# Performance work log

Hardware: AMD Instinct MI355X
Metric: run time of the kernel (lower is better)

Reference implementation:

```python
import jax, jax.numpy as jnp
import numpy as np

B, K, V, D, T = 8, 4, 32000, 1024, 16
EOS, PAD = 2, 0
EOS_SCORE = 1000.0
BIG = 1e9  # suppresses beams 1..K-1 at step 0 (original starts from a single beam)


def setup_inputs() -> dict:
    key = jax.random.key(0)
    k1, k2, k3, k4 = jax.random.split(key, 4)
    s = 1.0 / np.sqrt(D)
    return {
        "words": jnp.ones((B, K), dtype=jnp.int32),  # BOS=1 on every beam
        "h0": jnp.zeros((B, K, D), dtype=jnp.float32),
        "c0": jnp.zeros((B, K, D), dtype=jnp.float32),
        "E": jax.random.normal(k1, (V, D), dtype=jnp.float32) * s,
        "Wx": jax.random.normal(k2, (D, 4 * D), dtype=jnp.float32) * s,
        "Wh": jax.random.normal(k3, (D, 4 * D), dtype=jnp.float32) * s,
        "b": jnp.zeros((4 * D,), dtype=jnp.float32),
        "Wout": jax.random.normal(k4, (D, V), dtype=jnp.float32) * s,
        "bout": jnp.zeros((V,), dtype=jnp.float32),
    }


def reference(words, h0, c0, E, Wx, Wh, b, Wout, bout):
    bidx = jnp.arange(B)[:, None]
    kidx = jnp.arange(K)[None, :]
    scores0 = jnp.concatenate(
        [jnp.zeros((B, 1), jnp.float32), jnp.full((B, K - 1), BIG, jnp.float32)], axis=1)
    buf0 = jnp.zeros((B, K, T), dtype=jnp.int32)
    stopped0 = jnp.zeros((B,), dtype=bool)

    def step(carry, j):
        w, scores, h, c, stopped, buf = carry
        # proc_word: embed -> LSTM cell -> vocab logits (vectorized over B*K beams)
        x = E[w]                                              # [B,K,D]
        gates = jnp.einsum('bkd,df->bkf', x, Wx) + jnp.einsum('bkd,df->bkf', h, Wh) + b
        i_, f_, g_, o_ = jnp.split(gates, 4, axis=-1)
        c_new = jax.nn.sigmoid(f_) * c + jax.nn.sigmoid(i_) * jnp.tanh(g_)
        h_new = jax.nn.sigmoid(o_) * jnp.tanh(c_new)
        logits = jnp.einsum('bkd,dv->bkv', h_new, Wout) + bout  # [B,K,V]
        p = -jax.nn.log_softmax(logits, axis=-1)                # negative log-probs
        neg_ps, idxs = jax.lax.top_k(-p, K)                     # K smallest per beam
        cand = (-neg_ps) + scores[:, :, None]                   # [B,K,K]
        flat = cand.reshape(B, K * K)
        wflat = idxs.reshape(B, K * K)
        neg_sel, sel = jax.lax.top_k(-flat, K)                  # K smallest over all cands
        sel_scores = -neg_sel                                   # [B,K]
        prev = sel // K                                         # originating beam
        new_w = jnp.take_along_axis(wflat, sel, axis=1)
        eos = new_w == EOS
        first_eos = eos[:, 0] & (~stopped)                      # best cand is EOS -> stop
        pen = eos & (~first_eos[:, None]) & (~stopped[:, None]) # non-best EOS penalized
        sel_scores = jnp.where(pen, EOS_SCORE, sel_scores)
        tok = jnp.where(first_eos[:, None], EOS, new_w)
        tok = jnp.where(stopped[:, None], PAD, tok)
        prevb = jnp.where(stopped[:, None], kidx, prev)         # stopped rows keep order
        buf = buf[bidx, prevb]                                  # reorder beam histories
        buf = buf.at[:, :, j].set(tok.astype(jnp.int32))
        h_new = h_new[bidx, prev]                               # gather per-beam states
        c_new = c_new[bidx, prev]
        scores = jnp.where(stopped[:, None], scores, sel_scores)
        w = jnp.where(stopped[:, None], w, new_w.astype(w.dtype))
        stopped = stopped | first_eos
        return (w, scores, h_new, c_new, stopped, buf), None

    carry0 = (words, scores0, h0, c0, stopped0, buf0)
    (_, scores, _, _, _, buf), _ = jax.lax.scan(step, carry0, jnp.arange(T))
    return buf, scores
```

## Files before the change

### kernel.cpp

```cpp
#include <hip/hip_runtime.h>
#include <math.h>
#include <float.h>

namespace {

constexpr int Bb = 8, Kk = 4, BKn = 32, Dd = 1024, Ff = 4096, Vv = 32000, Tt = 16;
constexpr int GDS = 32, GDC = 32;
constexpr int LTW = 64;
constexpr int LNB = Vv / LTW;
constexpr int LCH = 32;
constexpr int LNCHH = 16;
constexpr int NVCH = LNB;
constexpr int EOSt = 2, PADt = 0;
constexpr float BIGf = 1e9f, EOSSf = 1000.0f;

constexpr size_t OFF_HTN = 0;
constexpr size_t OFF_CB0 = OFF_HTN + (size_t)Dd * BKn;
constexpr size_t OFF_CB1 = OFF_CB0 + (size_t)BKn * Dd;
constexpr size_t OFF_GP  = OFF_CB1 + (size_t)BKn * Dd;
constexpr size_t OFF_CS  = OFF_GP  + (size_t)GDS * BKn * Ff;
constexpr size_t OFF_SC  = OFF_CS  + (size_t)NVCH * BKn * 12;
constexpr size_t OFF_INT = OFF_SC  + BKn;
constexpr int IW = 0, ISTOP = 32, IPREV = 40, IBUFA = 72, IBUFB = IBUFA + Bb * Kk * Tt;

__device__ __forceinline__ void cp16(const float* g, float* l) {
  __builtin_amdgcn_global_load_lds(
      (const __attribute__((address_space(1))) void*)g,
      (__attribute__((address_space(3))) void*)l, 16, 0, 0);
}

__device__ inline void ins4(float v, int id, float tv[4], int ti[4]) {
#pragma unroll
  for (int r = 0; r < 4; r++) {
    bool better = (v > tv[r]) || (v == tv[r] && id < ti[r]);
    if (better) { float fv = tv[r]; int fi = ti[r]; tv[r] = v; ti[r] = id; v = fv; id = fi; }
  }
}

template <int STARTOFF>
__device__ inline void merge_top4(float tv[4], int ti[4], float ov[4], int oi[4]) {
#pragma unroll
  for (int r = 0; r < 4; r++) {
    float hv = tv[0]; int hi = ti[0];
    float m = hv;
    for (int off = STARTOFF; off; off >>= 1) m = fmaxf(m, __shfl_xor(m, off));
    int c = (hv == m) ? hi : 0x7fffffff;
    for (int off = STARTOFF; off; off >>= 1) c = min(c, __shfl_xor(c, off));
    if (hv == m && hi == c) {
      tv[0] = tv[1]; ti[0] = ti[1];
      tv[1] = tv[2]; ti[1] = ti[2];
      tv[2] = tv[3]; ti[2] = ti[3];
      tv[3] = -FLT_MAX; ti[3] = 0x7fffffff;
    }
    ov[r] = m; oi[r] = c;
  }
}

__global__ __launch_bounds__(256) void initK(const int* __restrict__ words,
    const float* __restrict__ h0, const float* __restrict__ c0,
    float* __restrict__ ws) {
  int* wsi = (int*)(ws + OFF_INT);
  if (blockIdx.x < 128) {
    int g = blockIdx.x * 256 + threadIdx.x;
    int d = g >> 5, bk = g & 31;
    ws[OFF_HTN + g] = h0[(size_t)bk * Dd + d];
    ws[OFF_CB0 + g] = c0[g];
  } else {
    int t = threadIdx.x;
    if (t < BKn) {
      ws[OFF_SC + t] = ((t & 3) == 0) ? 0.f : BIGf;
      wsi[IW + t] = words[t];
      wsi[IPREV + t] = t & 3;
    }
    if (t < Bb) wsi[ISTOP + t] = 0;
    for (int i = t; i < 2 * Bb * Kk * Tt; i += 256) wsi[IBUFA + i] = 0;
  }
}

__global__ __launch_bounds__(256) void gatesK(const float* __restrict__ Wx,
    const float* __restrict__ Wh, const float* __restrict__ E,
    const float* __restrict__ hTn, const int* __restrict__ wsi,
    float* __restrict__ Gp) {
  __shared__ float xs[GDC][BKn], hs[GDC][BKn];
  int tid = threadIdx.x;
  int d0 = blockIdx.y * GDC;
  {
    int bk = tid & 31, dq = tid >> 5;
    int w = wsi[IW + bk];
    int src = (bk & ~3) | wsi[IPREV + bk];
    const float* Erow = E + (size_t)w * Dd + d0;
#pragma unroll
    for (int k = 0; k < 4; k++) {
      int d = dq * 4 + k;
      xs[d][bk] = Erow[d];
      hs[d][bk] = hTn[(size_t)(d0 + d) * BKn + src];
    }
  }
  __syncthreads();
  int ct = tid & 31, bg = tid >> 5;
  int f0 = blockIdx.x * 128 + ct * 4;
  float acc[4][4];
#pragma unroll
  for (int c = 0; c < 4; c++)
#pragma unroll
    for (int i = 0; i < 4; i++) acc[c][i] = 0.f;
#pragma unroll 4
  for (int d = 0; d < GDC; ++d) {
    float4 wx = *(const float4*)(Wx + (size_t)(d0 + d) * Ff + f0);
    float4 wh = *(const float4*)(Wh + (size_t)(d0 + d) * Ff + f0);
    float4 x4 = *(const float4*)&xs[d][bg * 4];
    float4 h4 = *(const float4*)&hs[d][bg * 4];
    float xv[4] = {x4.x, x4.y, x4.z, x4.w};
    float hv[4] = {h4.x, h4.y, h4.z, h4.w};
    float wxc[4] = {wx.x, wx.y, wx.z, wx.w};
    float whc[4] = {wh.x, wh.y, wh.z, wh.w};
#pragma unroll
    for (int c = 0; c < 4; c++)
#pragma unroll
      for (int i = 0; i < 4; i++)
        acc[c][i] = fmaf(xv[i], wxc[c], fmaf(hv[i], whc[c], acc[c][i]));
  }
#pragma unroll
  for (int i = 0; i < 4; i++) {
    int bk = bg * 4 + i;
    float4 o = {acc[0][i], acc[1][i], acc[2][i], acc[3][i]};
    *(float4*)(Gp + ((size_t)blockIdx.y * BKn + bk) * Ff + f0) = o;
  }
}

__global__ __launch_bounds__(256) void lstmK(const float* __restrict__ bvec,
    const float* __restrict__ Gp, const float* __restrict__ cPrev,
    const int* __restrict__ wsi, float* __restrict__ cNew,
    float* __restrict__ hTn) {
  __shared__ float part[4][128];
  int bk = blockIdx.x;
  int dcl = threadIdx.x & 127;
  int half = threadIdx.x >> 7;
  int dc = blockIdx.y * 128 + dcl;
  float s[4] = {0.f, 0.f, 0.f, 0.f};
#pragma unroll 4
  for (int dsl = 0; dsl < 16; dsl++) {
    int ds = half * 16 + dsl;
    const float* row = Gp + ((size_t)ds * BKn + bk) * Ff;
#pragma unroll
    for (int g = 0; g < 4; g++) s[g] += row[(size_t)g * Dd + dc];
  }
  if (half == 1) {
#pragma unroll
    for (int g = 0; g < 4; g++) part[g][dcl] = s[g];
  }
  __syncthreads();
  if (half == 0) {
    float gi = s[0] + part[0][dcl] + bvec[dc];
    float gf = s[1] + part[1][dcl] + bvec[Dd + dc];
    float gg = s[2] + part[2][dcl] + bvec[2 * Dd + dc];
    float go = s[3] + part[3][dcl] + bvec[3 * Dd + dc];
    int src = (bk & ~3) | wsi[IPREV + bk];
    float c = cPrev[(size_t)src * Dd + dc];
    float si = 1.f / (1.f + expf(-gi));
    float sf = 1.f / (1.f + expf(-gf));
    float so = 1.f / (1.f + expf(-go));
    float tg = tanhf(gg);
    float cn = sf * c + si * tg;
    float hn = so * tanhf(cn);
    cNew[(size_t)bk * Dd + dc] = cn;
    hTn[(size_t)dc * BKn + bk] = hn;
  }
}

__global__ __launch_bounds__(256) void logitsAK(const float* __restrict__ Wo,
    const float* __restrict__ bo, const float* __restrict__ hTn,
    float* __restrict__ cs) {
  __shared__ float wb[2][3][LCH][LTW];
  __shared__ float hb[2][3][LCH][BKn];
  __shared__ float sd[BKn][LTW];
  int tid = threadIdx.x;
  int half = tid >> 7;
  int htid = tid & 127;
  int hw = htid >> 6;
  int lane = tid & 63;
  int cg = htid & 15;
  int bg = htid >> 4;
  size_t v0 = (size_t)blockIdx.x * LTW;
  int dh0 = half * 512;
  float acc[4][4];
#pragma unroll
  for (int c = 0; c < 4; c++)
#pragma unroll
    for (int i = 0; i < 4; i++) acc[c][i] = 0.f;

  float4 b4 = *(const float4*)(bo + v0 + cg * 4);

#define STAGE(CH, B)                                                           \
  {                                                                            \
    int d0_ = dh0 + (CH) * LCH;                                                \
    _Pragma("unroll") for (int i_ = 0; i_ < 4; i_++) {                         \
      int db_ = hw * 16 + i_ * 4;                                              \
      cp16(Wo + (size_t)(d0_ + db_ + (lane >> 4)) * Vv + v0 + (lane & 15) * 4, \
           &wb[half][B][db_][0]);                                              \
    }                                                                          \
    _Pragma("unroll") for (int j_ = 0; j_ < 2; j_++) {                         \
      int db_ = hw * 16 + j_ * 8;                                              \
      cp16(hTn + (size_t)(d0_ + db_ + (lane >> 3)) * BKn + (lane & 7) * 4,     \
           &hb[half][B][db_][0]);                                              \
    }                                                                          \
  }

  STAGE(0, 0)
  STAGE(1, 1)
  for (int k = 0; k < LNCHH; k++) {
    int b = k % 3;
    if (k + 2 < LNCHH) {
      STAGE(k + 2, (k + 2) % 3)
      asm volatile("s_waitcnt vmcnt(12)" ::: "memory");
    } else if (k + 1 < LNCHH) {
      asm volatile("s_waitcnt vmcnt(6)" ::: "memory");
    } else {
      asm volatile("s_waitcnt vmcnt(0)" ::: "memory");
    }
    __builtin_amdgcn_s_barrier();
#pragma unroll 8
    for (int d = 0; d < LCH; d++) {
      float4 w4 = *(const float4*)&wb[half][b][d][cg * 4];
      float4 h4 = *(const float4*)&hb[half][b][d][bg * 4];
      acc[0][0] = fmaf(w4.x, h4.x, acc[0][0]);
      acc[1][0] = fmaf(w4.y, h4.x, acc[1][0]);
      acc[2][0] = fmaf(w4.z, h4.x, acc[2][0]);
      acc[3][0] = fmaf(w4.w, h4.x, acc[3][0]);
      acc[0][1] = fmaf(w4.x, h4.y, acc[0][1]);
      acc[1][1] = fmaf(w4.y, h4.y, acc[1][1]);
      acc[2][1] = fmaf(w4.z, h4.y, acc[2][1]);
      acc[3][1] = fmaf(w4.w, h4.y, acc[3][1]);
      acc[0][2] = fmaf(w4.x, h4.z, acc[0][2]);
      acc[1][2] = fmaf(w4.y, h4.z, acc[1][2]);
      acc[2][2] = fmaf(w4.z, h4.z, acc[2][2]);
      acc[3][2] = fmaf(w4.w, h4.z, acc[3][2]);
      acc[0][3] = fmaf(w4.x, h4.w, acc[0][3]);
      acc[1][3] = fmaf(w4.y, h4.w, acc[1][3]);
      acc[2][3] = fmaf(w4.z, h4.w, acc[2][3]);
      acc[3][3] = fmaf(w4.w, h4.w, acc[3][3]);
    }
    __builtin_amdgcn_s_barrier();
  }
#undef STAGE

  if (half == 0) {
#pragma unroll
    for (int c = 0; c < 4; c++)
#pragma unroll
      for (int i = 0; i < 4; i++)
        sd[bg * 4 + i][cg * 4 + c] = acc[c][i] + ((const float*)&b4)[c];
  }
  __syncthreads();
  if (half == 1) {
#pragma unroll
    for (int c = 0; c < 4; c++)
#pragma unroll
      for (int i = 0; i < 4; i++)
        sd[bg * 4 + i][cg * 4 + c] += acc[c][i];
  }
  __syncthreads();

  int wid = tid >> 6;
  int i0 = (int)v0 + lane;
  for (int bb_ = 0; bb_ < 8; ++bb_) {
    int bk = wid * 8 + bb_;
    float v0f = sd[bk][lane];
    float m = v0f;
    for (int off = 32; off; off >>= 1) m = fmaxf(m, __shfl_xor(m, off));
    float se = expf(v0f - m);
    for (int off = 32; off; off >>= 1) se += __shfl_xor(se, off);
    float tv[4]; int ti[4];
#pragma unroll
    for (int r = 0; r < 4; r++) { tv[r] = -FLT_MAX; ti[r] = 0x7fffffff; }
    ins4(v0f, i0, tv, ti);
    float ov[4]; int oi[4];
    merge_top4<32>(tv, ti, ov, oi);
    if (lane == 0) {
      float* p = cs + ((size_t)blockIdx.x * BKn + bk) * 12;
      p[0] = m; p[1] = se;
#pragma unroll
      for (int r = 0; r < 4; r++) { p[2 + r] = ov[r]; p[6 + r] = __int_as_float(oi[r]); }
    }
  }
}

__global__ __launch_bounds__(1024) void redSelK(float* __restrict__ ws, int step) {
  __shared__ float bt_s[BKn][8];
  __shared__ int s_tok[BKn], s_prevb[BKn];
  int* wsi = (int*)(ws + OFF_INT);
  const float* cs = ws + OFF_CS;
  int tid = threadIdx.x;
  int wv = tid >> 6, lane = tid & 63;
  {
    int half = lane >> 5, l32 = lane & 31;
    int bk = wv * 2 + half;
    float tv[4]; int ti[4];
#pragma unroll
    for (int r = 0; r < 4; r++) { tv[r] = -FLT_MAX; ti[r] = 0x7fffffff; }
    float M = -FLT_MAX, ls = 0.f;
    for (int g = 0; g < 4; g++) {
      float4 pa[4], pb[4], pc[4];
      bool vv[4];
#pragma unroll
      for (int j = 0; j < 4; j++) {
        int c = l32 + 32 * (g * 4 + j);
        vv[j] = c < NVCH;
        const float* p = cs + ((size_t)c * BKn + bk) * 12;
        if (vv[j]) {
          pa[j] = *(const float4*)p;
          pb[j] = *(const float4*)(p + 4);
          pc[j] = *(const float4*)(p + 8);
        }
      }
#pragma unroll
      for (int j = 0; j < 4; j++) {
        if (vv[j]) {
          float cm = pa[j].x, csum = pa[j].y;
          if (cm > M) { ls *= expf(M - cm); M = cm; }
          ls += csum * expf(cm - M);
          ins4(pa[j].z, __float_as_int(pb[j].z), tv, ti);
          ins4(pa[j].w, __float_as_int(pb[j].w), tv, ti);
          ins4(pb[j].x, __float_as_int(pc[j].x), tv, ti);
          ins4(pb[j].y, __float_as_int(pc[j].y), tv, ti);
        }
      }
    }
    for (int off = 16; off; off >>= 1) {
      float Mo = __shfl_xor(M, off), lso = __shfl_xor(ls, off);
      float Mn = fmaxf(M, Mo);
      ls = ls * expf(M - Mn) + lso * expf(Mo - Mn);
      M = Mn;
    }
    float lse = M + logf(ls);
    float ov[4]; int oi[4];
    merge_top4<16>(tv, ti, ov, oi);
    if (l32 == 0) {
#pragma unroll
      for (int r = 0; r < 4; r++) {
        bt_s[bk][r] = lse - ov[r];
        bt_s[bk][4 + r] = __int_as_float(oi[r]);
      }
    }
  }
  __syncthreads();
  if (tid < Bb) {
    int b = tid;
    int st = wsi[ISTOP + b];
    float sc[4];
#pragma unroll
    for (int k = 0; k < 4; k++) sc[k] = ws[OFF_SC + b * 4 + k];
    float cval[16]; int ctok[16];
#pragma unroll
    for (int kb = 0; kb < 4; kb++)
#pragma unroll
      for (int r = 0; r < 4; r++) {
        cval[kb * 4 + r] = bt_s[b * 4 + kb][r] + sc[kb];
        ctok[kb * 4 + r] = __float_as_int(bt_s[b * 4 + kb][4 + r]);
      }
    float selS[4]; int selW[4], prevK[4];
    int usedMask = 0;
#pragma unroll
    for (int r = 0; r < 4; r++) {
      int best = -1; float bv = FLT_MAX;
#pragma unroll
      for (int t = 0; t < 16; t++) {
        if (!((usedMask >> t) & 1) && cval[t] < bv) { bv = cval[t]; best = t; }
      }
      usedMask |= 1 << best;
      int tok = 0;
#pragma unroll
      for (int t = 0; t < 16; t++) if (t == best) tok = ctok[t];
      selS[r] = bv; selW[r] = tok; prevK[r] = best >> 2;
    }
    bool eos[4];
#pragma unroll
    for (int r = 0; r < 4; r++) eos[r] = (selW[r] == EOSt);
    bool first = eos[0] && !st;
#pragma unroll
    for (int r = 0; r < 4; r++) if (eos[r] && !first && !st) selS[r] = EOSSf;
#pragma unroll
    for (int k = 0; k < 4; k++) {
      int tok = st ? PADt : (first ? EOSt : selW[k]);
      int pb  = st ? k : prevK[k];
      s_tok[b * 4 + k] = tok;
      s_prevb[b * 4 + k] = pb;
      if (!st) { ws[OFF_SC + b * 4 + k] = selS[k]; wsi[IW + b * 4 + k] = selW[k]; }
      wsi[IPREV + b * 4 + k] = prevK[k];
    }
    wsi[ISTOP + b] = (st || first) ? 1 : 0;
  }
  __syncthreads();
  if (tid < 512) {
    const int* br = wsi + (((step & 1) == 0) ? IBUFA : IBUFB);
    int* bw = wsi + (((step & 1) == 0) ? IBUFB : IBUFA);
    int bkk = tid >> 4, t = tid & 15;
    int pb = s_prevb[bkk];
    int src = ((bkk & ~3) | pb) * Tt + t;
    int val = br[src];
    if (t == step) val = s_tok[bkk];
    bw[tid] = val;
  }
}

__global__ __launch_bounds__(256) void outK(const float* __restrict__ ws,
                                            float* __restrict__ out) {
  const int* wsi = (const int*)(ws + OFF_INT);
  int g = blockIdx.x * 256 + threadIdx.x;
  if (g < Bb * Kk * Tt) {
    out[g] = (float)wsi[IBUFA + g];
  } else if (g < Bb * Kk * Tt + BKn) {
    out[g] = ws[OFF_SC + (g - Bb * Kk * Tt)];
  }
}

}

extern "C" void kernel_launch(void* const* d_in, const int* in_sizes, int n_in,
                              void* d_out, int out_size, void* d_ws, size_t ws_size,
                              hipStream_t stream) {
  (void)in_sizes; (void)n_in; (void)out_size; (void)ws_size;
  const int*   words = (const int*)d_in[0];
  const float* h0 = (const float*)d_in[1];
  const float* c0 = (const float*)d_in[2];
  const float* E  = (const float*)d_in[3];
  const float* Wx = (const float*)d_in[4];
  const float* Wh = (const float*)d_in[5];
  const float* bv = (const float*)d_in[6];
  const float* Wo = (const float*)d_in[7];
  const float* bo = (const float*)d_in[8];
  float* ws = (float*)d_ws;
  float* hTn = ws + OFF_HTN;
  float* cb0 = ws + OFF_CB0;
  float* cb1 = ws + OFF_CB1;
  float* Gp  = ws + OFF_GP;
  float* cs  = ws + OFF_CS;
  int*   wsi = (int*)(ws + OFF_INT);

  initK<<<129, 256, 0, stream>>>(words, h0, c0, ws);
  for (int j = 0; j < Tt; j++) {
    float* cPrev = (j & 1) ? cb1 : cb0;
    float* cNext = (j & 1) ? cb0 : cb1;
    gatesK<<<dim3(32, GDS), 256, 0, stream>>>(Wx, Wh, E, hTn, wsi, Gp);
    lstmK<<<dim3(32, 8), 256, 0, stream>>>(bv, Gp, cPrev, wsi, cNext, hTn);
    logitsAK<<<LNB, 256, 0, stream>>>(Wo, bo, hTn, cs);
    redSelK<<<1, 1024, 0, stream>>>(ws, j);
  }
  outK<<<3, 256, 0, stream>>>(ws, (float*)d_out);
}
```

Baseline: 1.780 ms.

## Repack Wout into per-tile contiguous blocks for logits kernel loads

```diff
diff --git a/kernel.cpp b/kernel.cpp
--- a/kernel.cpp
+++ b/kernel.cpp
@@ -22,6 +22,7 @@
 constexpr size_t OFF_SC  = OFF_CS  + (size_t)NVCH * BKn * 12;
 constexpr size_t OFF_INT = OFF_SC  + BKn;
 constexpr int IW = 0, ISTOP = 32, IPREV = 40, IBUFA = 72, IBUFB = IBUFA + Bb * Kk * Tt;
+constexpr size_t OFF_PWO = OFF_INT + 2048;
 
 __device__ __forceinline__ void cp16(const float* g, float* l) {
   __builtin_amdgcn_global_load_lds(
@@ -77,6 +78,33 @@
   }
 }
 
+__global__ __launch_bounds__(256) void packWoK(const float* __restrict__ Wo,
+                                               float* __restrict__ pwo) {
+  __shared__ float tile[32][256];
+  int t = threadIdx.x;
+  int v0 = blockIdx.x * 256;
+  int d0 = blockIdx.y * 32;
+  int rs = t >> 6;
+  int lane = t & 63;
+#pragma unroll
+  for (int p = 0; p < 8; p++) {
+    int r = p * 4 + rs;
+    *(float4*)&tile[r][lane * 4] =
+        *(const float4*)(Wo + (size_t)(d0 + r) * Vv + v0 + lane * 4);
+  }
+  __syncthreads();
+  int tb = rs;
+  int b = (v0 >> 6) + tb;
+  float* dst = pwo + ((size_t)b * Dd + d0) * 64;
+#pragma unroll
+  for (int p = 0; p < 8; p++) {
+    int off = p * 256 + lane * 4;
+    int dd = off >> 6;
+    int cc = off & 63;
+    *(float4*)(dst + off) = *(const float4*)&tile[dd][tb * 64 + cc];
+  }
+}
+
 __global__ __launch_bounds__(256) void gatesK(const float* __restrict__ Wx,
     const float* __restrict__ Wh, const float* __restrict__ E,
     const float* __restrict__ hTn, const int* __restrict__ wsi,
@@ -168,7 +196,7 @@
   }
 }
 
-__global__ __launch_bounds__(256) void logitsAK(const float* __restrict__ Wo,
+__global__ __launch_bounds__(256) void logitsAK(const float* __restrict__ pwo,
     const float* __restrict__ bo, const float* __restrict__ hTn,
     float* __restrict__ cs) {
   __shared__ float wb[2][3][LCH][LTW];
@@ -183,6 +211,7 @@
   int bg = htid >> 4;
   size_t v0 = (size_t)blockIdx.x * LTW;
   int dh0 = half * 512;
+  const float* wbase = pwo + (size_t)blockIdx.x * Dd * 64;
   float acc[4][4];
 #pragma unroll
   for (int c = 0; c < 4; c++)
@@ -196,8 +225,7 @@
     int d0_ = dh0 + (CH) * LCH;                                                \
     _Pragma("unroll") for (int i_ = 0; i_ < 4; i_++) {                         \
       int db_ = hw * 16 + i_ * 4;                                              \
-      cp16(Wo + (size_t)(d0_ + db_ + (lane >> 4)) * Vv + v0 + (lane & 15) * 4, \
-           &wb[half][B][db_][0]);                                              \
+      cp16(wbase + (size_t)(d0_ + db_) * 64 + lane * 4, &wb[half][B][db_][0]); \
     }                                                                          \
     _Pragma("unroll") for (int j_ = 0; j_ < 2; j_++) {                         \
       int db_ = hw * 16 + j_ * 8;                                              \
@@ -435,15 +463,17 @@
   float* cb1 = ws + OFF_CB1;
   float* Gp  = ws + OFF_GP;
   float* cs  = ws + OFF_CS;
+  float* pwo = ws + OFF_PWO;
   int*   wsi = (int*)(ws + OFF_INT);
 
   initK<<<129, 256, 0, stream>>>(words, h0, c0, ws);
+  packWoK<<<dim3(125, 32), 256, 0, stream>>>(Wo, pwo);
   for (int j = 0; j < Tt; j++) {
     float* cPrev = (j & 1) ? cb1 : cb0;
     float* cNext = (j & 1) ? cb0 : cb1;
     gatesK<<<dim3(32, GDS), 256, 0, stream>>>(Wx, Wh, E, hTn, wsi, Gp);
     lstmK<<<dim3(32, 8), 256, 0, stream>>>(bv, Gp, cPrev, wsi, cNext, hTn);
-    logitsAK<<<LNB, 256, 0, stream>>>(Wo, bo, hTn, cs);
+    logitsAK<<<LNB, 256, 0, stream>>>(pwo, bo, hTn, cs);
     redSelK<<<1, 1024, 0, stream>>>(ws, j);
   }
   outK<<<3, 256, 0, stream>>>(ws, (float*)d_out);
```

After: 1.836 ms. +3.1%, slower.
